# Kernel optimization log

Measured on AMD Instinct MI355X. Metric: run time of the kernel, lower is better.

## Reference

```python
import jax, jax.numpy as jnp
import numpy as np

N_DIMS = 1024
N_HEADS = 16
HEAD_DIM = N_DIMS // N_HEADS


def setup_inputs() -> dict:
    key = jax.random.key(0)
    k_x, k_wa, k_wp = jax.random.split(key, 3)
    x = jax.random.normal(k_x, (4, 2048, N_DIMS), dtype=jnp.float32)
    # nn.Linear weights stored [out, in]; apply as x @ W.T
    scale_a = 1.0 / np.sqrt(N_DIMS)
    w_attn = jax.random.uniform(k_wa, (3 * N_DIMS, N_DIMS), jnp.float32, -scale_a, scale_a)
    w_proj = jax.random.uniform(k_wp, (N_DIMS, N_DIMS), jnp.float32, -scale_a, scale_a)
    return {"x": x, "w_attn": w_attn, "w_proj": w_proj}


def reference(x, w_attn, w_proj):
    B, S, D = x.shape
    qkv = x @ w_attn.T                                  # [B, S, 3D]
    q, k, v = jnp.split(qkv, 3, axis=-1)
    # [B, H, S, Dh]
    def heads(t):
        return t.reshape(B, S, N_HEADS, HEAD_DIM).transpose(0, 2, 1, 3)
    q, k, v = heads(q), heads(k), heads(v)
    scores = jnp.einsum('bhqd,bhkd->bhqk', q, k) * (1.0 / np.sqrt(HEAD_DIM))
    causal = jnp.tril(jnp.ones((S, S), dtype=bool))
    scores = jnp.where(causal[None, None], scores, -jnp.inf)
    attn = jax.nn.softmax(scores, axis=-1)              # dropout: eval mode (identity)
    y = jnp.einsum('bhqk,bhkd->bhqd', attn, v)
    y = y.transpose(0, 2, 1, 3).reshape(B, S, D)
    return y @ w_proj.T
```

## Files before the change

kernel.cpp:

```cpp
#include <hip/hip_runtime.h>

typedef unsigned short ushort_t;
typedef __attribute__((ext_vector_type(8))) short bf16x8;
typedef __attribute__((ext_vector_type(4))) float f32x4;


__device__ __forceinline__ ushort_t f2bf(float f) {
    union { float f; unsigned u; } c; c.f = f;
    unsigned u = c.u;
    unsigned r = (u + 0x7fffu + ((u >> 16) & 1u)) >> 16;
    return (ushort_t)r;
}

__device__ __forceinline__ ushort_t f2bf_fast(float f) {
    union { float f; unsigned u; } c; c.f = f;
    return (ushort_t)((c.u + 0x8000u) >> 16);
}

__device__ __forceinline__ void gld_lds16(const ushort_t* g, ushort_t* l) {
    __builtin_amdgcn_global_load_lds(
        (const __attribute__((address_space(1))) void*)g,
        (__attribute__((address_space(3))) void*)l, 16, 0, 0);
}

template <int CTRL>
__device__ __forceinline__ float dpp_f32(float x) {
    int r = __builtin_amdgcn_update_dpp(0, __builtin_bit_cast(int, x), CTRL, 0xF, 0xF, true);
    return __builtin_bit_cast(float, r);
}
__device__ __forceinline__ float rsum16(float x) {
    x += dpp_f32<0xB1>(x);
    x += dpp_f32<0x4E>(x);
    x += dpp_f32<0x141>(x);
    x += dpp_f32<0x140>(x);
    return x;
}


__global__ void convert_bf16(const float* __restrict__ in, ushort_t* __restrict__ out, int n4) {
    int i = blockIdx.x * blockDim.x + threadIdx.x;
    if (i < n4) {
        const float4 f = ((const float4*)in)[i];
        ushort4 o;
        o.x = f2bf(f.x); o.y = f2bf(f.y); o.z = f2bf(f.z); o.w = f2bf(f.w);
        ((ushort4*)out)[i] = o;
    }
}


__global__ __launch_bounds__(256) void gemm_qkv(
    const ushort_t* __restrict__ A, const ushort_t* __restrict__ W,
    ushort_t* __restrict__ qo, ushort_t* __restrict__ ko, ushort_t* __restrict__ vto)
{
    constexpr int K = 1024;
    const int m0 = blockIdx.x * 128;
    const int n0 = blockIdx.y * 128;
    __shared__ alignas(16) ushort_t smem[8192];
    ushort_t* sA = smem;
    ushort_t* sB = smem + 4096;
    const int tid = threadIdx.x;
    const int wave = tid >> 6, lane = tid & 63;
    const int quad = lane >> 4, l16 = lane & 15;
    const int wm = (wave >> 1) << 6, wn = (wave & 1) << 6;
    const int srow = lane >> 2;
    const int scol = (((lane & 3) ^ ((srow >> 1) & 3)) << 3);
    const int fg = ((quad ^ ((l16 >> 1) & 3)) << 3);

    f32x4 acc[4][4] = {};
    const ushort_t* aRow0 = A + (size_t)(m0 + wave * 32 + srow) * K + scol;
    const ushort_t* bRow0 = W + (size_t)(n0 + wave * 32 + srow) * K + scol;

    for (int k0 = 0; k0 < K; k0 += 32) {
#pragma unroll
        for (int c = 0; c < 2; ++c) {
            gld_lds16(aRow0 + (size_t)c * 16 * K + k0, sA + (wave * 2 + c) * 512);
            gld_lds16(bRow0 + (size_t)c * 16 * K + k0, sB + (wave * 2 + c) * 512);
        }
        __syncthreads();
        bf16x8 af[4], bfr[4];
#pragma unroll
        for (int f = 0; f < 4; ++f) {
            af[f]  = *(const bf16x8*)(sA + (wm + f * 16 + l16) * 32 + fg);
            bfr[f] = *(const bf16x8*)(sB + (wn + f * 16 + l16) * 32 + fg);
        }
#pragma unroll
        for (int mf = 0; mf < 4; ++mf)
#pragma unroll
            for (int nf = 0; nf < 4; ++nf)
                acc[mf][nf] = __builtin_amdgcn_mfma_f32_16x16x32_bf16(af[mf], bfr[nf], acc[mf][nf], 0, 0, 0);
        __syncthreads();
    }

    const int which = n0 >> 10;
    ushort_t* sT = smem + wave * 2048;
    const int b  = (m0 + wm) >> 11;
    const int sb = (m0 + wm) & 2047;
    const int h  = ((n0 + wn) & 1023) >> 6;
    const int bh = b * 16 + h;

    if (which < 2) {
        ushort_t* go = (which == 0) ? qo : ko;
        const float qs1 = (which == 0) ? 0.18033688011112042f : 1.0f;
#pragma unroll
        for (int mf = 0; mf < 4; ++mf) {
#pragma unroll
            for (int nf = 0; nf < 4; ++nf)
#pragma unroll
                for (int i = 0; i < 4; ++i) {
                    const int mll = quad * 4 + i;
                    sT[mll * 64 + ((nf * 16 + l16) ^ (4 * (mll & 7)))] = f2bf(acc[mf][nf][i] * qs1);
                }
            __builtin_amdgcn_s_waitcnt(0);
#pragma unroll
            for (int p = 0; p < 4; ++p) {
                const int mll = p * 4 + quad;
                const ushort4 val = *(const ushort4*)(sT + mll * 64 + ((l16 * 4) ^ (4 * (mll & 7))));
                const int s = sb + mf * 16 + mll;
                *(ushort4*)(go + ((size_t)bh * 2048 + s) * 64 + l16 * 4) = val;
            }
            __builtin_amdgcn_s_waitcnt(0);
        }
    } else {
#pragma unroll
        for (int nf = 0; nf < 4; ++nf) {
#pragma unroll
            for (int mf = 0; mf < 4; ++mf) {
                ushort4 w;
                w.x = f2bf(acc[mf][nf][0]);
                w.y = f2bf(acc[mf][nf][1]);
                w.z = f2bf(acc[mf][nf][2]);
                w.w = f2bf(acc[mf][nf][3]);
                *(ushort4*)(sT + l16 * 64 + ((mf * 16 + quad * 4) ^ (4 * (l16 & 7)))) = w;
            }
            __builtin_amdgcn_s_waitcnt(0);
#pragma unroll
            for (int p = 0; p < 4; ++p) {
                const int nll = p * 4 + quad;
                const ushort4 val = *(const ushort4*)(sT + nll * 64 + ((l16 * 4) ^ (4 * (nll & 7))));
                const int dh = nf * 16 + nll;
                *(ushort4*)(vto + ((size_t)bh * 64 + dh) * 2048 + sb + l16 * 4) = val;
            }
            __builtin_amdgcn_s_waitcnt(0);
        }
    }
}


template <bool MASK>
__device__ __forceinline__ void softmax_tile(
    const f32x4 (&sacc)[2][4], float (&lpart)[2][4], ushort_t* sPw,
    int wrmin, int k0, int quad, int l16, int l8)
{
#pragma unroll
    for (int mf = 0; mf < 2; ++mf)
#pragma unroll
        for (int nf = 0; nf < 4; ++nf)
#pragma unroll
            for (int i = 0; i < 4; ++i) {
                float sv = sacc[mf][nf][i];
                if (MASK) {
                    const int rg = wrmin + mf * 16 + quad * 4 + i;
                    const int cg = k0 + nf * 16 + l16;
                    sv = (cg <= rg) ? sv : -3.0e38f;
                }
                const float p = __builtin_amdgcn_exp2f(sv);
                lpart[mf][i] += p;
                const int pr = mf * 16 + quad * 4 + i;
                const int grp = (nf * 2 + (l16 >> 3)) ^ (pr & 7);
                sPw[pr * 64 + grp * 8 + l8] = f2bf_fast(p);
            }
}

__global__ __launch_bounds__(256) void attn(
    const ushort_t* __restrict__ qg_, const ushort_t* __restrict__ kg_,
    const ushort_t* __restrict__ vg_, ushort_t* __restrict__ y)
{
    const int bh = blockIdx.x;
    int qy = blockIdx.y;
    qy = (qy & 4) ? ((qy & 8) ? 27 - qy : 11 - qy) : qy;
    const int q0 = qy * 128;
    const int b = bh >> 4, h = bh & 15;
    const int tid = threadIdx.x, wave = tid >> 6, lane = tid & 63;
    const int quad = lane >> 4, l16 = lane & 15;
    const int l8 = lane & 7;

    __shared__ alignas(16) ushort_t sQP[128 * 64];
    __shared__ alignas(16) ushort_t sK[64 * 64];
    __shared__ alignas(16) ushort_t sV[64 * 64];

    const ushort_t* qg = qg_ + ((size_t)bh * 2048 + q0) * 64;
    const ushort_t* kg = kg_ + (size_t)bh * 2048 * 64;
    const ushort_t* vg = vg_ + (size_t)bh * 64 * 2048;

    {
        const int row = lane >> 3, e = l8 << 3;
#pragma unroll
        for (int c = 0; c < 4; ++c) {
            const int chunk = wave * 4 + c;
            gld_lds16(qg + (size_t)(chunk * 8 + row) * 64 + e, sQP + chunk * 512);
        }
    }
    __syncthreads();

    bf16x8 aq[2][2];
#pragma unroll
    for (int mf = 0; mf < 2; ++mf)
#pragma unroll
        for (int ks = 0; ks < 2; ++ks)
            aq[mf][ks] = *(const bf16x8*)(sQP + (wave * 32 + mf * 16 + l16) * 64 + ks * 32 + quad * 8);

    f32x4 oacc[2][4] = {};
    float lpart[2][4] = {};

    const int ktiles = 2 * qy + 2;
    const int srow8 = lane >> 3;
    const int sg = ((l8 ^ srow8) << 3);
    const int wrmin = q0 + wave * 32, wrmax = wrmin + 31;
    ushort_t* sPw = sQP + wave * 2048;

    for (int t = 0; t < ktiles; ++t) {
        const int k0 = t * 64;
        __syncthreads();
#pragma unroll
        for (int c = 0; c < 2; ++c) {
            const int chunk = wave * 2 + c;
            gld_lds16(kg + (size_t)(k0 + chunk * 8 + srow8) * 64 + sg, sK + chunk * 512);
            gld_lds16(vg + (size_t)(chunk * 8 + srow8) * 2048 + k0 + sg, sV + chunk * 512);
        }
        __syncthreads();
        if (k0 > wrmax) continue;

        f32x4 sacc[2][4] = {};
#pragma unroll
        for (int ks = 0; ks < 2; ++ks) {
            bf16x8 bk[4];
#pragma unroll
            for (int nf = 0; nf < 4; ++nf)
                bk[nf] = *(const bf16x8*)(sK + (nf * 16 + l16) * 64 + (((ks * 4 + quad) ^ (l16 & 7)) << 3));
#pragma unroll
            for (int mf = 0; mf < 2; ++mf)
#pragma unroll
                for (int nf = 0; nf < 4; ++nf)
                    sacc[mf][nf] = __builtin_amdgcn_mfma_f32_16x16x32_bf16(aq[mf][ks], bk[nf], sacc[mf][nf], 0, 0, 0);
        }

        if (k0 + 63 > wrmin)
            softmax_tile<true>(sacc, lpart, sPw, wrmin, k0, quad, l16, l8);
        else
            softmax_tile<false>(sacc, lpart, sPw, wrmin, k0, quad, l16, l8);

#pragma unroll
        for (int ks = 0; ks < 2; ++ks) {
            bf16x8 pa[2], vb[4];
            const int rgrp = ((ks * 4 + quad) ^ (l16 & 7)) << 3;
#pragma unroll
            for (int mf = 0; mf < 2; ++mf)
                pa[mf] = *(const bf16x8*)(sPw + (mf * 16 + l16) * 64 + rgrp);
#pragma unroll
            for (int nf = 0; nf < 4; ++nf)
                vb[nf] = *(const bf16x8*)(sV + (nf * 16 + l16) * 64 + rgrp);
#pragma unroll
            for (int mf = 0; mf < 2; ++mf)
#pragma unroll
                for (int nf = 0; nf < 4; ++nf)
                    oacc[mf][nf] = __builtin_amdgcn_mfma_f32_16x16x32_bf16(pa[mf], vb[nf], oacc[mf][nf], 0, 0, 0);
        }
    }

#pragma unroll
    for (int mf = 0; mf < 2; ++mf) {
#pragma unroll
        for (int i = 0; i < 4; ++i) {
            const float inv = 1.0f / rsum16(lpart[mf][i]);
            const int r = q0 + wave * 32 + mf * 16 + quad * 4 + i;
#pragma unroll
            for (int nf = 0; nf < 4; ++nf)
                y[((size_t)b * 2048 + r) * 1024 + h * 64 + nf * 16 + l16] =
                    f2bf(oacc[mf][nf][i] * inv);
        }
    }
}


__global__ __launch_bounds__(256) void gemm_proj(
    const ushort_t* __restrict__ A, const ushort_t* __restrict__ W, float* __restrict__ out)
{
    constexpr int K = 1024;
    const int m0 = blockIdx.x * 128;
    const int n0 = blockIdx.y * 128;
    __shared__ alignas(16) ushort_t sA[128 * 32];
    __shared__ alignas(16) ushort_t sB[128 * 32];
    const int tid = threadIdx.x;
    const int wave = tid >> 6, lane = tid & 63;
    const int quad = lane >> 4, l16 = lane & 15;
    const int wm = (wave >> 1) << 6, wn = (wave & 1) << 6;
    const int srow = lane >> 2;
    const int scol = (((lane & 3) ^ ((srow >> 1) & 3)) << 3);
    const int fg = ((quad ^ ((l16 >> 1) & 3)) << 3);

    f32x4 acc[4][4] = {};
    const ushort_t* aRow0 = A + (size_t)(m0 + wave * 32 + srow) * K + scol;
    const ushort_t* bRow0 = W + (size_t)(n0 + wave * 32 + srow) * K + scol;

    for (int k0 = 0; k0 < K; k0 += 32) {
#pragma unroll
        for (int c = 0; c < 2; ++c) {
            gld_lds16(aRow0 + (size_t)c * 16 * K + k0, sA + (wave * 2 + c) * 512);
            gld_lds16(bRow0 + (size_t)c * 16 * K + k0, sB + (wave * 2 + c) * 512);
        }
        __syncthreads();
        bf16x8 af[4], bfr[4];
#pragma unroll
        for (int f = 0; f < 4; ++f) {
            af[f]  = *(const bf16x8*)(sA + (wm + f * 16 + l16) * 32 + fg);
            bfr[f] = *(const bf16x8*)(sB + (wn + f * 16 + l16) * 32 + fg);
        }
#pragma unroll
        for (int mf = 0; mf < 4; ++mf)
#pragma unroll
            for (int nf = 0; nf < 4; ++nf)
                acc[mf][nf] = __builtin_amdgcn_mfma_f32_16x16x32_bf16(af[mf], bfr[nf], acc[mf][nf], 0, 0, 0);
        __syncthreads();
    }

#pragma unroll
    for (int mf = 0; mf < 4; ++mf)
#pragma unroll
        for (int nf = 0; nf < 4; ++nf)
#pragma unroll
            for (int i = 0; i < 4; ++i) {
                const int m = m0 + wm + mf * 16 + quad * 4 + i;
                const int n = n0 + wn + nf * 16 + l16;
                out[(size_t)m * 1024 + n] = acc[mf][nf][i];
            }
}


extern "C" void kernel_launch(void* const* d_in, const int* in_sizes, int n_in,
                              void* d_out, int out_size, void* d_ws, size_t ws_size,
                              hipStream_t stream) {
    const float* x  = (const float*)d_in[0];
    const float* wa = (const float*)d_in[1];
    const float* wp = (const float*)d_in[2];
    float* out = (float*)d_out;

    char* ws = (char*)d_ws;
    ushort_t* xb  = (ushort_t*)(ws);
    ushort_t* wab = (ushort_t*)(ws + 16777216);
    ushort_t* wpb = (ushort_t*)(ws + 16777216 + 6291456);
    ushort_t* q   = (ushort_t*)(ws + 25165824);
    ushort_t* k   = (ushort_t*)(ws + 41943040);
    ushort_t* vt  = (ushort_t*)(ws + 58720256);
    ushort_t* y   = xb;

    convert_bf16<<<8192 * 1024 / 4 / 256, 256, 0, stream>>>(x, xb, 8192 * 1024 / 4);
    convert_bf16<<<3072 * 1024 / 4 / 256, 256, 0, stream>>>(wa, wab, 3072 * 1024 / 4);
    convert_bf16<<<1024 * 1024 / 4 / 256, 256, 0, stream>>>(wp, wpb, 1024 * 1024 / 4);

    gemm_qkv<<<dim3(64, 24), 256, 0, stream>>>(xb, wab, q, k, vt);
    attn<<<dim3(64, 16), 256, 0, stream>>>(q, k, vt, y);
    gemm_proj<<<dim3(64, 8), 256, 0, stream>>>(y, wpb, out);
}
```

Measured before the change: 257.2 us.

## Pair causal query tiles per block and compute transposed S to pack P stores

The attention grid is halved so each block runs two passes over query tiles qy and 15-qy, which evens out causal work per block in place of the earlier index-permutation trick. The QK^T product is computed transposed (K as the A operand), so each lane holds four consecutive key columns. P can then be packed into 64-bit LDS stores rather than scalar 16-bit writes, and row sums reduce with two cross-lane shuffles instead of a DPP chain. The trade-off is fewer blocks in flight (512) and a serial second pass per block, which may hurt occupancy and latency hiding.

After: 257.5 us. About the same (+0.1%).

```diff
diff --git a/kernel.cpp b/kernel.cpp
--- a/kernel.cpp
+++ b/kernel.cpp
@@ -12,28 +12,14 @@
     return (ushort_t)r;
 }
 
-__device__ __forceinline__ ushort_t f2bf_fast(float f) {
-    union { float f; unsigned u; } c; c.f = f;
-    return (ushort_t)((c.u + 0x8000u) >> 16);
+__device__ __forceinline__ unsigned fbits(float f) {
+    union { float f; unsigned u; } c; c.f = f; return c.u;
 }
 
 __device__ __forceinline__ void gld_lds16(const ushort_t* g, ushort_t* l) {
     __builtin_amdgcn_global_load_lds(
         (const __attribute__((address_space(1))) void*)g,
         (__attribute__((address_space(3))) void*)l, 16, 0, 0);
-}
-
-template <int CTRL>
-__device__ __forceinline__ float dpp_f32(float x) {
-    int r = __builtin_amdgcn_update_dpp(0, __builtin_bit_cast(int, x), CTRL, 0xF, 0xF, true);
-    return __builtin_bit_cast(float, r);
-}
-__device__ __forceinline__ float rsum16(float x) {
-    x += dpp_f32<0xB1>(x);
-    x += dpp_f32<0x4E>(x);
-    x += dpp_f32<0x141>(x);
-    x += dpp_f32<0x140>(x);
-    return x;
 }
 
 
@@ -146,39 +132,11 @@
 }
 
 
-template <bool MASK>
-__device__ __forceinline__ void softmax_tile(
-    const f32x4 (&sacc)[2][4], float (&lpart)[2][4], ushort_t* sPw,
-    int wrmin, int k0, int quad, int l16, int l8)
-{
-#pragma unroll
-    for (int mf = 0; mf < 2; ++mf)
-#pragma unroll
-        for (int nf = 0; nf < 4; ++nf)
-#pragma unroll
-            for (int i = 0; i < 4; ++i) {
-                float sv = sacc[mf][nf][i];
-                if (MASK) {
-                    const int rg = wrmin + mf * 16 + quad * 4 + i;
-                    const int cg = k0 + nf * 16 + l16;
-                    sv = (cg <= rg) ? sv : -3.0e38f;
-                }
-                const float p = __builtin_amdgcn_exp2f(sv);
-                lpart[mf][i] += p;
-                const int pr = mf * 16 + quad * 4 + i;
-                const int grp = (nf * 2 + (l16 >> 3)) ^ (pr & 7);
-                sPw[pr * 64 + grp * 8 + l8] = f2bf_fast(p);
-            }
-}
-
 __global__ __launch_bounds__(256) void attn(
     const ushort_t* __restrict__ qg_, const ushort_t* __restrict__ kg_,
     const ushort_t* __restrict__ vg_, ushort_t* __restrict__ y)
 {
     const int bh = blockIdx.x;
-    int qy = blockIdx.y;
-    qy = (qy & 4) ? ((qy & 8) ? 27 - qy : 11 - qy) : qy;
-    const int q0 = qy * 128;
     const int b = bh >> 4, h = bh & 15;
     const int tid = threadIdx.x, wave = tid >> 6, lane = tid & 63;
     const int quad = lane >> 4, l16 = lane & 15;
@@ -188,95 +146,130 @@
     __shared__ alignas(16) ushort_t sK[64 * 64];
     __shared__ alignas(16) ushort_t sV[64 * 64];
 
-    const ushort_t* qg = qg_ + ((size_t)bh * 2048 + q0) * 64;
     const ushort_t* kg = kg_ + (size_t)bh * 2048 * 64;
     const ushort_t* vg = vg_ + (size_t)bh * 64 * 2048;
 
-    {
-        const int row = lane >> 3, e = l8 << 3;
-#pragma unroll
-        for (int c = 0; c < 4; ++c) {
-            const int chunk = wave * 4 + c;
-            gld_lds16(qg + (size_t)(chunk * 8 + row) * 64 + e, sQP + chunk * 512);
-        }
-    }
-    __syncthreads();
-
-    bf16x8 aq[2][2];
-#pragma unroll
-    for (int mf = 0; mf < 2; ++mf)
-#pragma unroll
-        for (int ks = 0; ks < 2; ++ks)
-            aq[mf][ks] = *(const bf16x8*)(sQP + (wave * 32 + mf * 16 + l16) * 64 + ks * 32 + quad * 8);
-
-    f32x4 oacc[2][4] = {};
-    float lpart[2][4] = {};
-
-    const int ktiles = 2 * qy + 2;
     const int srow8 = lane >> 3;
     const int sg = ((l8 ^ srow8) << 3);
-    const int wrmin = q0 + wave * 32, wrmax = wrmin + 31;
     ushort_t* sPw = sQP + wave * 2048;
 
-    for (int t = 0; t < ktiles; ++t) {
-        const int k0 = t * 64;
-        __syncthreads();
-#pragma unroll
-        for (int c = 0; c < 2; ++c) {
-            const int chunk = wave * 2 + c;
-            gld_lds16(kg + (size_t)(k0 + chunk * 8 + srow8) * 64 + sg, sK + chunk * 512);
-            gld_lds16(vg + (size_t)(chunk * 8 + srow8) * 2048 + k0 + sg, sV + chunk * 512);
-        }
-        __syncthreads();
-        if (k0 > wrmax) continue;
-
-        f32x4 sacc[2][4] = {};
-#pragma unroll
-        for (int ks = 0; ks < 2; ++ks) {
-            bf16x8 bk[4];
-#pragma unroll
-            for (int nf = 0; nf < 4; ++nf)
-                bk[nf] = *(const bf16x8*)(sK + (nf * 16 + l16) * 64 + (((ks * 4 + quad) ^ (l16 & 7)) << 3));
-#pragma unroll
-            for (int mf = 0; mf < 2; ++mf)
+    for (int pass = 0; pass < 2; ++pass) {
+        const int qy = pass ? (15 - (int)blockIdx.y) : (int)blockIdx.y;
+        const int q0 = qy * 128;
+        const ushort_t* qg = qg_ + ((size_t)bh * 2048 + q0) * 64;
+
+        __syncthreads();
+        {
+            const int row = lane >> 3, e = l8 << 3;
+#pragma unroll
+            for (int c = 0; c < 4; ++c) {
+                const int chunk = wave * 4 + c;
+                gld_lds16(qg + (size_t)(chunk * 8 + row) * 64 + e, sQP + chunk * 512);
+            }
+        }
+        __syncthreads();
+
+        bf16x8 bq[2][2];
+#pragma unroll
+        for (int qf = 0; qf < 2; ++qf)
+#pragma unroll
+            for (int ks = 0; ks < 2; ++ks)
+                bq[qf][ks] = *(const bf16x8*)(sQP + (wave * 32 + qf * 16 + l16) * 64 + ks * 32 + quad * 8);
+
+        f32x4 oacc[2][4] = {};
+        float lpart[2] = {0.f, 0.f};
+
+        const int ktiles = 2 * qy + 2;
+        const int wrmin = q0 + wave * 32, wrmax = wrmin + 31;
+
+        for (int t = 0; t < ktiles; ++t) {
+            const int k0 = t * 64;
+            __syncthreads();
+#pragma unroll
+            for (int c = 0; c < 2; ++c) {
+                const int chunk = wave * 2 + c;
+                gld_lds16(kg + (size_t)(k0 + chunk * 8 + srow8) * 64 + sg, sK + chunk * 512);
+                gld_lds16(vg + (size_t)(chunk * 8 + srow8) * 2048 + k0 + sg, sV + chunk * 512);
+            }
+            __syncthreads();
+            if (k0 > wrmax) continue;
+
+            f32x4 sacc[4][2] = {};
+#pragma unroll
+            for (int ks = 0; ks < 2; ++ks) {
+                bf16x8 ak[4];
+#pragma unroll
+                for (int kf = 0; kf < 4; ++kf)
+                    ak[kf] = *(const bf16x8*)(sK + (kf * 16 + l16) * 64 + (((ks * 4 + quad) ^ l8) << 3));
+#pragma unroll
+                for (int kf = 0; kf < 4; ++kf)
+#pragma unroll
+                    for (int qf = 0; qf < 2; ++qf)
+                        sacc[kf][qf] = __builtin_amdgcn_mfma_f32_16x16x32_bf16(ak[kf], bq[qf][ks], sacc[kf][qf], 0, 0, 0);
+            }
+
+            const bool diag = (k0 + 63 > wrmin);
+#pragma unroll
+            for (int kf = 0; kf < 4; ++kf) {
+#pragma unroll
+                for (int qf = 0; qf < 2; ++qf) {
+                    float p[4];
+#pragma unroll
+                    for (int i = 0; i < 4; ++i) {
+                        float sv = sacc[kf][qf][i];
+                        if (diag) {
+                            const int cg = k0 + kf * 16 + quad * 4 + i;
+                            const int rg = wrmin + qf * 16 + l16;
+                            sv = (cg <= rg) ? sv : -3.0e38f;
+                        }
+                        p[i] = __builtin_amdgcn_exp2f(sv);
+                        lpart[qf] += p[i];
+                    }
+                    uint2 w;
+                    w.x = ((fbits(p[0]) + 0x8000u) >> 16) | ((fbits(p[1]) + 0x8000u) & 0xffff0000u);
+                    w.y = ((fbits(p[2]) + 0x8000u) >> 16) | ((fbits(p[3]) + 0x8000u) & 0xffff0000u);
+                    *(uint2*)(sPw + (qf * 16 + l16) * 64 +
+                              (((kf * 2 + (quad >> 1)) ^ l8) << 3) + ((quad & 1) << 2)) = w;
+                }
+            }
+
+#pragma unroll
+            for (int ks = 0; ks < 2; ++ks) {
+                bf16x8 pa[2], vb[4];
+                const int rgrp = (((ks * 4 + quad) ^ l8) << 3);
+#pragma unroll
+                for (int mf = 0; mf < 2; ++mf)
+                    pa[mf] = *(const bf16x8*)(sPw + (mf * 16 + l16) * 64 + rgrp);
 #pragma unroll
                 for (int nf = 0; nf < 4; ++nf)
-                    sacc[mf][nf] = __builtin_amdgcn_mfma_f32_16x16x32_bf16(aq[mf][ks], bk[nf], sacc[mf][nf], 0, 0, 0);
-        }
-
-        if (k0 + 63 > wrmin)
-            softmax_tile<true>(sacc, lpart, sPw, wrmin, k0, quad, l16, l8);
-        else
-            softmax_tile<false>(sacc, lpart, sPw, wrmin, k0, quad, l16, l8);
-
-#pragma unroll
-        for (int ks = 0; ks < 2; ++ks) {
-            bf16x8 pa[2], vb[4];
-            const int rgrp = ((ks * 4 + quad) ^ (l16 & 7)) << 3;
-#pragma unroll
-            for (int mf = 0; mf < 2; ++mf)
-                pa[mf] = *(const bf16x8*)(sPw + (mf * 16 + l16) * 64 + rgrp);
-#pragma unroll
-            for (int nf = 0; nf < 4; ++nf)
-                vb[nf] = *(const bf16x8*)(sV + (nf * 16 + l16) * 64 + rgrp);
-#pragma unroll
-            for (int mf = 0; mf < 2; ++mf)
+                    vb[nf] = *(const bf16x8*)(sV + (nf * 16 + l16) * 64 + rgrp);
+#pragma unroll
+                for (int mf = 0; mf < 2; ++mf)
+#pragma unroll
+                    for (int nf = 0; nf < 4; ++nf)
+                        oacc[mf][nf] = __builtin_amdgcn_mfma_f32_16x16x32_bf16(pa[mf], vb[nf], oacc[mf][nf], 0, 0, 0);
+            }
+        }
+
+        float rl[2];
+#pragma unroll
+        for (int qf = 0; qf < 2; ++qf) {
+            float x = lpart[qf];
+            x += __shfl_xor(x, 16);
+            x += __shfl_xor(x, 32);
+            rl[qf] = x;
+        }
+#pragma unroll
+        for (int mf = 0; mf < 2; ++mf) {
+#pragma unroll
+            for (int i = 0; i < 4; ++i) {
+                const float inv = 1.0f / __shfl(rl[mf], quad * 4 + i);
+                const int r = q0 + wave * 32 + mf * 16 + quad * 4 + i;
 #pragma unroll
                 for (int nf = 0; nf < 4; ++nf)
-                    oacc[mf][nf] = __builtin_amdgcn_mfma_f32_16x16x32_bf16(pa[mf], vb[nf], oacc[mf][nf], 0, 0, 0);
-        }
-    }
-
-#pragma unroll
-    for (int mf = 0; mf < 2; ++mf) {
-#pragma unroll
-        for (int i = 0; i < 4; ++i) {
-            const float inv = 1.0f / rsum16(lpart[mf][i]);
-            const int r = q0 + wave * 32 + mf * 16 + quad * 4 + i;
-#pragma unroll
-            for (int nf = 0; nf < 4; ++nf)
-                y[((size_t)b * 2048 + r) * 1024 + h * 64 + nf * 16 + l16] =
-                    f2bf(oacc[mf][nf][i] * inv);
+                    y[((size_t)b * 2048 + r) * 1024 + h * 64 + nf * 16 + l16] =
+                        f2bf(oacc[mf][nf][i] * inv);
+            }
         }
     }
 }
@@ -358,6 +351,6 @@
     convert_bf16<<<1024 * 1024 / 4 / 256, 256, 0, stream>>>(wp, wpb, 1024 * 1024 / 4);
 
     gemm_qkv<<<dim3(64, 24), 256, 0, stream>>>(xb, wab, q, k, vt);
-    attn<<<dim3(64, 16), 256, 0, stream>>>(q, k, vt, y);
+    attn<<<dim3(64, 8), 256, 0, stream>>>(q, k, vt, y);
     gemm_proj<<<dim3(64, 8), 256, 0, stream>>>(y, wpb, out);
 }
```
